# Optimization experiments

Hardware: AMD Instinct MI355X
Metric: run time of the kernel (lower is better)

Reference implementation:

```python
import jax, jax.numpy as jnp
import numpy as np

N = 50000
E = 800000
IN_C = 64
OUT_C = 128
T = 4


def setup_inputs() -> dict:
    key = jax.random.key(0)
    ks = jax.random.split(key, 12)
    s = 0.05
    return {
        "x": jax.random.normal(ks[0], (N, IN_C), dtype=jnp.float32),
        "u": jax.random.normal(ks[1], (N, OUT_C), dtype=jnp.float32),
        "edge_index": jax.random.randint(ks[2], (2, E), 0, N, dtype=jnp.int32),
        # w1: Linear(in_channels, out_channels)
        "w1_W": jax.random.normal(ks[3], (OUT_C, IN_C), dtype=jnp.float32) * s,
        "w1_b": jnp.zeros((OUT_C,), dtype=jnp.float32),
        # sigmod MLP: three Linear(out, out) layers
        "m1_W": jax.random.normal(ks[4], (OUT_C, OUT_C), dtype=jnp.float32) * s,
        "m1_b": jnp.zeros((OUT_C,), dtype=jnp.float32),
        "m2_W": jax.random.normal(ks[5], (OUT_C, OUT_C), dtype=jnp.float32) * s,
        "m2_b": jnp.zeros((OUT_C,), dtype=jnp.float32),
        "m3_W": jax.random.normal(ks[6], (OUT_C, OUT_C), dtype=jnp.float32) * s,
        "m3_b": jnp.zeros((OUT_C,), dtype=jnp.float32),
        # w2: Linear(out, out) for graph readout
        "w2_W": jax.random.normal(ks[7], (OUT_C, OUT_C), dtype=jnp.float32) * s,
        "w2_b": jnp.zeros((OUT_C,), dtype=jnp.float32),
    }


def reference(x, u, edge_index, w1_W, w1_b, m1_W, m1_b, m2_W, m2_b, m3_W, m3_b, w2_W, w2_b):
    n_nodes = x.shape[0]
    src = edge_index[0]  # gather source (u_j)
    dst = edge_index[1]  # scatter-add target
    xw = x @ w1_W.T + w1_b  # [N, out]; identical every iteration
    for _ in range(T):
        agg = jax.ops.segment_sum(u[src], dst, num_segments=n_nodes)  # [N, out]
        h = jax.nn.relu(agg @ m1_W.T + m1_b)
        h = jax.nn.relu(h @ m2_W.T + m2_b)
        h = jnp.tanh(h @ m3_W.T + m3_b)
        u = jax.nn.relu(xw + h)
    g = jnp.sum(u, axis=0, keepdims=True)  # e @ u with e = ones [1, N]
    return g @ w2_W.T + w2_b  # [1, out]
```

## Files before the change

kernel.cpp:

```cpp
#include <hip/hip_runtime.h>
#include <hip/hip_bf16.h>

#define NN 50000
#define NE 800000
#define CI 64
#define CO 128
#define SCANB 49

typedef __attribute__((ext_vector_type(8))) short bf16x8;
typedef __attribute__((ext_vector_type(4))) float f32x4;

__device__ __forceinline__ unsigned short f2bf(float f) {
  unsigned int u = __float_as_uint(f);
  u += 0x7fffu + ((u >> 16) & 1u);
  return (unsigned short)(u >> 16);
}
__device__ __forceinline__ float bf2f_lo(unsigned int p) { return __uint_as_float(p << 16); }
__device__ __forceinline__ float bf2f_hi(unsigned int p) { return __uint_as_float(p & 0xffff0000u); }
__device__ __forceinline__ unsigned int pk2(float lo, float hi) {
  return ((unsigned int)f2bf(hi) << 16) | (unsigned int)f2bf(lo);
}

__global__ void k_count(const int* __restrict__ dst, int* __restrict__ deg) {
  int e = blockIdx.x * blockDim.x + threadIdx.x;
  if (e < NE) atomicAdd(&deg[dst[e]], 1);
}

__global__ __launch_bounds__(256) void k_scan1(const int* __restrict__ deg, int* __restrict__ bsum) {
  int i0 = blockIdx.x * 1024 + threadIdx.x * 4;
  int s = 0;
#pragma unroll
  for (int j = 0; j < 4; ++j) { int i = i0 + j; if (i < NN) s += deg[i]; }
#pragma unroll
  for (int off = 32; off; off >>= 1) s += __shfl_down(s, off);
  __shared__ int ws[4];
  if ((threadIdx.x & 63) == 0) ws[threadIdx.x >> 6] = s;
  __syncthreads();
  if (threadIdx.x == 0) bsum[blockIdx.x] = ws[0] + ws[1] + ws[2] + ws[3];
}

__global__ __launch_bounds__(64) void k_scan2(const int* __restrict__ bsum, int* __restrict__ boff) {
  int t = threadIdx.x;
  int v = (t < SCANB) ? bsum[t] : 0;
  int incl = v;
#pragma unroll
  for (int off = 1; off < 64; off <<= 1) {
    int o = __shfl_up(incl, off);
    if (t >= off) incl += o;
  }
  if (t < SCANB) boff[t] = incl - v;
}

__global__ __launch_bounds__(256) void k_scan3(const int* __restrict__ deg, const int* __restrict__ boff,
                                               int* __restrict__ row_off) {
  int b = blockIdx.x;
  int i0 = b * 1024 + threadIdx.x * 4;
  int v[4]; int tsum = 0;
#pragma unroll
  for (int j = 0; j < 4; ++j) { int i = i0 + j; v[j] = (i < NN) ? deg[i] : 0; tsum += v[j]; }
  int incl = tsum;
#pragma unroll
  for (int off = 1; off < 64; off <<= 1) {
    int o = __shfl_up(incl, off);
    if ((threadIdx.x & 63) >= (unsigned)off) incl += o;
  }
  __shared__ int ws[4];
  int w = threadIdx.x >> 6;
  if ((threadIdx.x & 63) == 63) ws[w] = incl;
  __syncthreads();
  int wbase = 0;
  for (int k = 0; k < 4; ++k) if (k < w) wbase += ws[k];
  int excl = boff[b] + wbase + incl - tsum;
#pragma unroll
  for (int j = 0; j < 4; ++j) { int i = i0 + j; if (i < NN) row_off[i] = excl; excl += v[j]; }
  if (b == 0 && threadIdx.x == 0) row_off[NN] = NE;
}

__global__ void k_fill(const int* __restrict__ src, const int* __restrict__ dst,
                       const int* __restrict__ row_off, int* __restrict__ cursor,
                       int* __restrict__ ssrc) {
  int e = blockIdx.x * blockDim.x + threadIdx.x;
  if (e < NE) {
    int d = dst[e];
    int pos = atomicAdd(&cursor[d], 1);
    ssrc[row_off[d] + pos] = src[e];
  }
}

__global__ void k_cvt_w(const float* __restrict__ w1, const float* __restrict__ m1,
                        const float* __restrict__ m2, const float* __restrict__ m3,
                        unsigned short* __restrict__ o) {
  int i = blockIdx.x * blockDim.x + threadIdx.x;
  if (i >= 57344) return;
  float v;
  if (i < 8192) v = w1[i];
  else if (i < 24576) v = m1[i - 8192];
  else if (i < 40960) v = m2[i - 24576];
  else v = m3[i - 40960];
  o[i] = f2bf(v);
}

__global__ void k_cvt4(const float* __restrict__ in, unsigned short* __restrict__ out, int n4) {
  int i = blockIdx.x * blockDim.x + threadIdx.x;
  if (i >= n4) return;
  float4 v = *(const float4*)(in + i * 4);
  ushort2 lo = { f2bf(v.x), f2bf(v.y) };
  ushort2 hi = { f2bf(v.z), f2bf(v.w) };
  *(ushort2*)(out + i * 4) = lo;
  *(ushort2*)(out + i * 4 + 2) = hi;
}

__global__ __launch_bounds__(256) void k_gather(const int* __restrict__ row_off,
    const int* __restrict__ ssrc, const unsigned short* __restrict__ ubf,
    unsigned short* __restrict__ agg) {
  int node = blockIdx.x * 4 + (threadIdx.x >> 6);
  if (node >= NN) return;
  int lane = threadIdx.x & 63;
  int eg = lane >> 4, c = lane & 15;
  int beg = row_off[node], end = row_off[node + 1];
  float a[8];
#pragma unroll
  for (int i = 0; i < 8; ++i) a[i] = 0.f;

#define ADD8(r) { a[0] += bf2f_lo(r.x); a[1] += bf2f_hi(r.x); \
                  a[2] += bf2f_lo(r.y); a[3] += bf2f_hi(r.y); \
                  a[4] += bf2f_lo(r.z); a[5] += bf2f_hi(r.z); \
                  a[6] += bf2f_lo(r.w); a[7] += bf2f_hi(r.w); }

  for (int base = beg; base < end; base += 64) {
    int e = base + lane;
    int sid = (e < end) ? ssrc[e] : 0;
    int cnt = min(64, end - base);
    int j = 0;
    for (; j + 16 <= cnt; j += 16) {
      int s0 = __shfl(sid, j + 0 + eg);
      int s1 = __shfl(sid, j + 4 + eg);
      int s2 = __shfl(sid, j + 8 + eg);
      int s3 = __shfl(sid, j + 12 + eg);
      uint4 r0 = *(const uint4*)(ubf + (size_t)s0 * CO + c * 8);
      uint4 r1 = *(const uint4*)(ubf + (size_t)s1 * CO + c * 8);
      uint4 r2 = *(const uint4*)(ubf + (size_t)s2 * CO + c * 8);
      uint4 r3 = *(const uint4*)(ubf + (size_t)s3 * CO + c * 8);
      ADD8(r0); ADD8(r1); ADD8(r2); ADD8(r3);
    }
    for (; j + 4 <= cnt; j += 4) {
      int s = __shfl(sid, j + eg);
      uint4 r = *(const uint4*)(ubf + (size_t)s * CO + c * 8);
      ADD8(r);
    }
    if (j < cnt) {
      int rem = cnt - j;
      int s = __shfl(sid, j + min(eg, rem - 1));
      if (eg < rem) {
        uint4 r = *(const uint4*)(ubf + (size_t)s * CO + c * 8);
        ADD8(r);
      }
    }
  }
#undef ADD8
#pragma unroll
  for (int i = 0; i < 8; ++i) { a[i] += __shfl_xor(a[i], 16); a[i] += __shfl_xor(a[i], 32); }
  if (lane < 16) {
    uint4 o;
    o.x = pk2(a[0], a[1]); o.y = pk2(a[2], a[3]);
    o.z = pk2(a[4], a[5]); o.w = pk2(a[6], a[7]);
    *(uint4*)(agg + (size_t)node * CO + c * 8) = o;
  }
}

__global__ __launch_bounds__(256) void k_xw(const unsigned short* __restrict__ A,
    const unsigned short* __restrict__ W, const float* __restrict__ bias,
    unsigned short* __restrict__ xwb) {
  int wave = threadIdx.x >> 6, lane = threadIdx.x & 63;
  int m = lane & 15, q = lane >> 4;
  int row0 = blockIdx.x * 64 + wave * 16;
  int arow = row0 + m; if (arow >= NN) arow = NN - 1;
  const unsigned short* Ar = A + (size_t)arow * CI;
  f32x4 acc[8];
#pragma unroll
  for (int tt = 0; tt < 8; ++tt) acc[tt] = (f32x4){0.f, 0.f, 0.f, 0.f};
#pragma unroll
  for (int ks = 0; ks < CI; ks += 32) {
    bf16x8 a = *(const bf16x8*)(Ar + ks + q * 8);
#pragma unroll
    for (int tt = 0; tt < 8; ++tt) {
      bf16x8 b = *(const bf16x8*)(W + (size_t)(tt * 16 + m) * CI + ks + q * 8);
      acc[tt] = __builtin_amdgcn_mfma_f32_16x16x32_bf16(a, b, acc[tt], 0, 0, 0);
    }
  }
#pragma unroll
  for (int tt = 0; tt < 8; ++tt) {
    int o = tt * 16 + m;
    float bv = bias[o];
#pragma unroll
    for (int r = 0; r < 4; ++r) {
      int node = row0 + q * 4 + r;
      if (node < NN) xwb[(size_t)node * CO + o] = f2bf(acc[tt][r] + bv);
    }
  }
}

__global__ __launch_bounds__(512, 4) void k_mlp(const unsigned short* __restrict__ agg,
    const unsigned short* __restrict__ W1, const unsigned short* __restrict__ W2,
    const unsigned short* __restrict__ W3,
    const float* __restrict__ b1, const float* __restrict__ b2, const float* __restrict__ b3,
    const unsigned short* __restrict__ xwb, unsigned short* __restrict__ uout) {
  constexpr int SP = 136;
  __shared__ unsigned short lds[16384 + 8 * 16 * SP];
  unsigned short* wt = lds;
  int tid = threadIdx.x;
  int wave = tid >> 6, lane = tid & 63;
  int m = lane & 15, q = lane >> 4;
  int row0 = blockIdx.x * 128 + wave * 16;
  unsigned short* L = lds + 16384 + wave * 16 * SP;
  int ar = row0 + m; if (ar >= NN) ar = NN - 1;
  const unsigned short* Ap = agg + (size_t)ar * CO;

  uint4 wreg[4];
  const int trb = (tid >> 4) & 7;
  const int tc  = tid & 15;
  const int ldst0 = (tid >> 4) * 128 + ((tc ^ trb) << 3);
  auto stage_load = [&](const unsigned short* W) {
#pragma unroll
    for (int j = 0; j < 4; ++j)
      wreg[j] = *(const uint4*)(W + ((j * 512 + tid) << 3));
  };
  auto stage_write = [&]() {
#pragma unroll
    for (int j = 0; j < 4; ++j)
      *(uint4*)(wt + ldst0 + j * 4096) = wreg[j];
  };
  auto bfrag = [&](int t, int ks) -> bf16x8 {
    int ch = (ks >> 3) + q;
    return *(const bf16x8*)(wt + (t * 16 + m) * 128 + ((ch ^ (m & 7)) << 3));
  };

  stage_load(W1);
  bf16x8 ar4[4];
#pragma unroll
  for (int k4 = 0; k4 < 4; ++k4) ar4[k4] = *(const bf16x8*)(Ap + k4 * 32 + q * 8);
  stage_write();

  f32x4 acc[8];
#pragma unroll
  for (int t = 0; t < 8; ++t) acc[t] = (f32x4){0.f, 0.f, 0.f, 0.f};
  __syncthreads();

#pragma unroll
  for (int k4 = 0; k4 < 4; ++k4) {
#pragma unroll
    for (int t = 0; t < 8; ++t) {
      bf16x8 b = bfrag(t, k4 * 32);
      acc[t] = __builtin_amdgcn_mfma_f32_16x16x32_bf16(ar4[k4], b, acc[t], 0, 0, 0);
    }
  }
  stage_load(W2);
#pragma unroll
  for (int t = 0; t < 8; ++t) {
    float bv = b1[t * 16 + m];
#pragma unroll
    for (int r = 0; r < 4; ++r)
      L[(q * 4 + r) * SP + t * 16 + m] = f2bf(fmaxf(acc[t][r] + bv, 0.f));
  }
  __syncthreads();
  stage_write();
#pragma unroll
  for (int t = 0; t < 8; ++t) acc[t] = (f32x4){0.f, 0.f, 0.f, 0.f};
  __syncthreads();

#pragma unroll
  for (int ks = 0; ks < CO; ks += 32) {
    bf16x8 a = *(const bf16x8*)(L + m * SP + ks + q * 8);
#pragma unroll
    for (int t = 0; t < 8; ++t) {
      bf16x8 b = bfrag(t, ks);
      acc[t] = __builtin_amdgcn_mfma_f32_16x16x32_bf16(a, b, acc[t], 0, 0, 0);
    }
  }
  stage_load(W3);
#pragma unroll
  for (int t = 0; t < 8; ++t) {
    float bv = b2[t * 16 + m];
#pragma unroll
    for (int r = 0; r < 4; ++r)
      L[(q * 4 + r) * SP + t * 16 + m] = f2bf(fmaxf(acc[t][r] + bv, 0.f));
  }
  __syncthreads();
  stage_write();
#pragma unroll
  for (int t = 0; t < 8; ++t) acc[t] = (f32x4){0.f, 0.f, 0.f, 0.f};
  __syncthreads();

#pragma unroll
  for (int ks = 0; ks < CO; ks += 32) {
    bf16x8 a = *(const bf16x8*)(L + m * SP + ks + q * 8);
#pragma unroll
    for (int t = 0; t < 8; ++t) {
      bf16x8 b = bfrag(t, ks);
      acc[t] = __builtin_amdgcn_mfma_f32_16x16x32_bf16(a, b, acc[t], 0, 0, 0);
    }
  }
#pragma unroll
  for (int t = 0; t < 8; ++t) {
    float bv = b3[t * 16 + m];
#pragma unroll
    for (int r = 0; r < 4; ++r) {
      float v = acc[t][r] + bv;
      float e = __expf(2.f * v);
      v = 1.f - 2.f / (e + 1.f);
      L[(q * 4 + r) * SP + t * 16 + m] = f2bf(v);
    }
  }
  int ln = lane >> 2, lc = lane & 3;
  int gnode = row0 + ln;
  if (gnode < NN) {
    const unsigned short* xr = xwb + (size_t)gnode * CO;
    unsigned short* ur = uout + (size_t)gnode * CO;
#pragma unroll
    for (int rnd = 0; rnd < 4; ++rnd) {
      int ch = (rnd * 4 + lc) * 8;
      uint4 h = *(const uint4*)(L + ln * SP + ch);
      uint4 xv = *(const uint4*)(xr + ch);
      uint4 o;
      o.x = pk2(fmaxf(bf2f_lo(h.x) + bf2f_lo(xv.x), 0.f), fmaxf(bf2f_hi(h.x) + bf2f_hi(xv.x), 0.f));
      o.y = pk2(fmaxf(bf2f_lo(h.y) + bf2f_lo(xv.y), 0.f), fmaxf(bf2f_hi(h.y) + bf2f_hi(xv.y), 0.f));
      o.z = pk2(fmaxf(bf2f_lo(h.z) + bf2f_lo(xv.z), 0.f), fmaxf(bf2f_hi(h.z) + bf2f_hi(xv.z), 0.f));
      o.w = pk2(fmaxf(bf2f_lo(h.w) + bf2f_lo(xv.w), 0.f), fmaxf(bf2f_hi(h.w) + bf2f_hi(xv.w), 0.f));
      *(uint4*)(ur + ch) = o;
    }
  }
}

__global__ __launch_bounds__(256) void k_reduce(const unsigned short* __restrict__ u,
                                                float* __restrict__ g) {
  int ch2 = threadIdx.x & 63;
  int sub = threadIdx.x >> 6;
  float a0 = 0.f, a1 = 0.f;
  for (int n = blockIdx.x * 4 + sub; n < NN; n += gridDim.x * 4) {
    unsigned int p = *(const unsigned int*)(u + (size_t)n * CO + ch2 * 2);
    a0 += bf2f_lo(p); a1 += bf2f_hi(p);
  }
  __shared__ float s0[256], s1[256];
  s0[threadIdx.x] = a0; s1[threadIdx.x] = a1;
  __syncthreads();
  if (sub == 0) {
    a0 = s0[ch2] + s0[64 + ch2] + s0[128 + ch2] + s0[192 + ch2];
    a1 = s1[ch2] + s1[64 + ch2] + s1[128 + ch2] + s1[192 + ch2];
    atomicAdd(&g[ch2 * 2], a0);
    atomicAdd(&g[ch2 * 2 + 1], a1);
  }
}

__global__ void k_final(const float* __restrict__ g, const float* __restrict__ w2,
                        const float* __restrict__ b2, float* __restrict__ outp) {
  __shared__ float sg[128];
  if (threadIdx.x < 128) sg[threadIdx.x] = g[threadIdx.x];
  __syncthreads();
  int j = threadIdx.x;
  if (j < 128) {
    float acc = b2[j];
    for (int c = 0; c < 128; ++c) acc += sg[c] * w2[j * 128 + c];
    outp[j] = acc;
  }
}

extern "C" void kernel_launch(void* const* d_in, const int* in_sizes, int n_in,
                              void* d_out, int out_size, void* d_ws, size_t ws_size,
                              hipStream_t stream) {
  (void)in_sizes; (void)n_in; (void)out_size; (void)ws_size;
  const float* x   = (const float*)d_in[0];
  const float* u0  = (const float*)d_in[1];
  const int*   ei  = (const int*)d_in[2];
  const float* w1W = (const float*)d_in[3];
  const float* w1b = (const float*)d_in[4];
  const float* m1W = (const float*)d_in[5];
  const float* m1b = (const float*)d_in[6];
  const float* m2W = (const float*)d_in[7];
  const float* m2b = (const float*)d_in[8];
  const float* m3W = (const float*)d_in[9];
  const float* m3b = (const float*)d_in[10];
  const float* w2W = (const float*)d_in[11];
  const float* w2b = (const float*)d_in[12];
  const int* esrc = ei;
  const int* edst = ei + NE;

  char* p = (char*)d_ws;
  auto carve = [&](size_t bytes) { char* r = p; p += (bytes + 255) & ~(size_t)255; return r; };
  unsigned short* xwb     = (unsigned short*)carve((size_t)NN * CO * 2);
  unsigned short* ubf     = (unsigned short*)carve((size_t)NN * CO * 2);
  unsigned short* agg     = (unsigned short*)carve((size_t)NN * CO * 2);
  unsigned short* xb      = (unsigned short*)carve((size_t)NN * CI * 2);
  unsigned short* wbf     = (unsigned short*)carve((size_t)57344 * 2);
  int*            row_off = (int*)carve((size_t)(NN + 1) * 4);
  int*            deg     = (int*)carve((size_t)NN * 4);
  int*            cursor  = (int*)carve((size_t)NN * 4);
  int*            ssrc    = (int*)carve((size_t)NE * 4);
  int*            bsum    = (int*)carve((size_t)SCANB * 4);
  int*            boff    = (int*)carve((size_t)SCANB * 4);
  float*          g       = (float*)carve(128 * 4);

  hipMemsetAsync(deg, 0, (size_t)NN * 4, stream);
  hipMemsetAsync(cursor, 0, (size_t)NN * 4, stream);
  hipMemsetAsync(g, 0, 128 * 4, stream);

  k_count<<<(NE + 255) / 256, 256, 0, stream>>>(edst, deg);
  k_scan1<<<SCANB, 256, 0, stream>>>(deg, bsum);
  k_scan2<<<1, 64, 0, stream>>>(bsum, boff);
  k_scan3<<<SCANB, 256, 0, stream>>>(deg, boff, row_off);
  k_fill<<<(NE + 255) / 256, 256, 0, stream>>>(esrc, edst, row_off, cursor, ssrc);
  k_cvt_w<<<(57344 + 255) / 256, 256, 0, stream>>>(w1W, m1W, m2W, m3W, wbf);
  k_cvt4<<<(NN * CI / 4 + 255) / 256, 256, 0, stream>>>(x, xb, NN * CI / 4);
  k_cvt4<<<(NN * CO / 4 + 255) / 256, 256, 0, stream>>>(u0, ubf, NN * CO / 4);

  k_xw<<<(NN + 63) / 64, 256, 0, stream>>>(xb, wbf, w1b, xwb);

  const unsigned short* Wm1 = wbf + 8192;
  const unsigned short* Wm2 = wbf + 8192 + 16384;
  const unsigned short* Wm3 = wbf + 8192 + 2 * 16384;
  const int GM = (NN + 127) / 128;
  for (int it = 0; it < 4; ++it) {
    k_gather<<<(NN + 3) / 4, 256, 0, stream>>>(row_off, ssrc, ubf, agg);
    k_mlp<<<GM, 512, 0, stream>>>(agg, Wm1, Wm2, Wm3, m1b, m2b, m3b, xwb, ubf);
  }

  k_reduce<<<256, 256, 0, stream>>>(ubf, g);
  k_final<<<1, 128, 0, stream>>>(g, w2W, w2b, (float*)d_out);
}
```

Baseline: 450.1 us.

## Build CSR via two-level bucketing with LDS atomics instead of global atomics

Replaces the global-atomic degree count and scatter fill with a bucketed approach. Edges are first binned into 196 buckets of 256 destination nodes each, using block-local histograms and LDS atomics. Per-bucket kernels then compute degrees and fill the CSR source array using shared-memory counters. This removes contended and random global atomics, at the cost of more kernel launches, an extra pairs buffer, and low parallelism (196 blocks) in the per-bucket kernels.

```diff
diff --git a/kernel.cpp b/kernel.cpp
--- a/kernel.cpp
+++ b/kernel.cpp
@@ -6,6 +6,9 @@
 #define CI 64
 #define CO 128
 #define SCANB 49
+#define NB 196
+#define CHUNK 2048
+#define NCH 391
 
 typedef __attribute__((ext_vector_type(8))) short bf16x8;
 typedef __attribute__((ext_vector_type(4))) float f32x4;
@@ -21,9 +24,86 @@
   return ((unsigned int)f2bf(hi) << 16) | (unsigned int)f2bf(lo);
 }
 
-__global__ void k_count(const int* __restrict__ dst, int* __restrict__ deg) {
-  int e = blockIdx.x * blockDim.x + threadIdx.x;
-  if (e < NE) atomicAdd(&deg[dst[e]], 1);
+
+__global__ __launch_bounds__(256) void k_bhist(const int* __restrict__ dst,
+                                               int* __restrict__ bcnt) {
+  __shared__ int lc[NB];
+  int tid = threadIdx.x;
+  for (int t = tid; t < NB; t += 256) lc[t] = 0;
+  __syncthreads();
+  int base = blockIdx.x * CHUNK;
+#pragma unroll
+  for (int i = 0; i < 8; ++i) {
+    int idx = base + i * 256 + tid;
+    if (idx < NE) atomicAdd(&lc[dst[idx] >> 8], 1);
+  }
+  __syncthreads();
+  for (int t = tid; t < NB; t += 256) if (lc[t]) atomicAdd(&bcnt[t], lc[t]);
+}
+
+__global__ __launch_bounds__(256) void k_bscan(const int* __restrict__ bcnt,
+                                               int* __restrict__ bkt_off,
+                                               int* __restrict__ bkt_cur) {
+  __shared__ int s[256];
+  int t = threadIdx.x;
+  int v = (t < NB) ? bcnt[t] : 0;
+  s[t] = v;
+  __syncthreads();
+  for (int off = 1; off < 256; off <<= 1) {
+    int x = (t >= off) ? s[t - off] : 0;
+    __syncthreads();
+    s[t] += x;
+    __syncthreads();
+  }
+  if (t < NB) { int e = s[t] - v; bkt_off[t] = e; bkt_cur[t] = e; }
+  if (t == 0) bkt_off[NB] = NE;
+}
+
+__global__ __launch_bounds__(256) void k_bin(const int* __restrict__ src,
+                                             const int* __restrict__ dst,
+                                             int* __restrict__ bkt_cur,
+                                             uint2* __restrict__ pairs) {
+  __shared__ int lcnt[NB];
+  __shared__ int lbase[NB];
+  int tid = threadIdx.x;
+  for (int t = tid; t < NB; t += 256) lcnt[t] = 0;
+  __syncthreads();
+  int base = blockIdx.x * CHUNK;
+  int ds[8], sr[8], rk[8];
+#pragma unroll
+  for (int i = 0; i < 8; ++i) {
+    int idx = base + i * 256 + tid;
+    if (idx < NE) {
+      ds[i] = dst[idx]; sr[i] = src[idx];
+      rk[i] = atomicAdd(&lcnt[ds[i] >> 8], 1);
+    } else ds[i] = -1;
+  }
+  __syncthreads();
+  for (int t = tid; t < NB; t += 256)
+    lbase[t] = lcnt[t] ? atomicAdd(&bkt_cur[t], lcnt[t]) : 0;
+  __syncthreads();
+#pragma unroll
+  for (int i = 0; i < 8; ++i) {
+    if (ds[i] >= 0) {
+      uint2 pr; pr.x = (unsigned)sr[i]; pr.y = (unsigned)ds[i];
+      pairs[lbase[ds[i] >> 8] + rk[i]] = pr;
+    }
+  }
+}
+
+__global__ __launch_bounds__(256) void k_deg(const uint2* __restrict__ pairs,
+                                             const int* __restrict__ bkt_off,
+                                             int* __restrict__ deg) {
+  __shared__ int lc[256];
+  int t = threadIdx.x, b = blockIdx.x;
+  lc[t] = 0;
+  __syncthreads();
+  int beg = bkt_off[b], end = bkt_off[b + 1];
+  for (int i = beg + t; i < end; i += 256)
+    atomicAdd(&lc[pairs[i].y & 255], 1);
+  __syncthreads();
+  int node = (b << 8) + t;
+  if (node < NN) deg[node] = lc[t];
 }
 
 __global__ __launch_bounds__(256) void k_scan1(const int* __restrict__ deg, int* __restrict__ bsum) {
@@ -76,14 +156,20 @@
   if (b == 0 && threadIdx.x == 0) row_off[NN] = NE;
 }
 
-__global__ void k_fill(const int* __restrict__ src, const int* __restrict__ dst,
-                       const int* __restrict__ row_off, int* __restrict__ cursor,
-                       int* __restrict__ ssrc) {
-  int e = blockIdx.x * blockDim.x + threadIdx.x;
-  if (e < NE) {
-    int d = dst[e];
-    int pos = atomicAdd(&cursor[d], 1);
-    ssrc[row_off[d] + pos] = src[e];
+__global__ __launch_bounds__(256) void k_fillB(const uint2* __restrict__ pairs,
+                                               const int* __restrict__ bkt_off,
+                                               const int* __restrict__ row_off,
+                                               int* __restrict__ ssrc) {
+  __shared__ int lcur[256];
+  int t = threadIdx.x, b = blockIdx.x;
+  lcur[t] = 0;
+  __syncthreads();
+  int beg = bkt_off[b], end = bkt_off[b + 1];
+  for (int i = beg + t; i < end; i += 256) {
+    uint2 e = pairs[i];
+    int d = (int)e.y;
+    int pos = row_off[d] + atomicAdd(&lcur[d & 255], 1);
+    ssrc[pos] = (int)e.x;
   }
 }
 
@@ -393,21 +479,27 @@
   unsigned short* wbf     = (unsigned short*)carve((size_t)57344 * 2);
   int*            row_off = (int*)carve((size_t)(NN + 1) * 4);
   int*            deg     = (int*)carve((size_t)NN * 4);
-  int*            cursor  = (int*)carve((size_t)NN * 4);
   int*            ssrc    = (int*)carve((size_t)NE * 4);
+  uint2*          pairs   = (uint2*)carve((size_t)NE * 8);
+  int*            bkt_cnt = (int*)carve((size_t)NB * 4);
+  int*            bkt_off = (int*)carve((size_t)(NB + 1) * 4);
+  int*            bkt_cur = (int*)carve((size_t)NB * 4);
   int*            bsum    = (int*)carve((size_t)SCANB * 4);
   int*            boff    = (int*)carve((size_t)SCANB * 4);
   float*          g       = (float*)carve(128 * 4);
 
-  hipMemsetAsync(deg, 0, (size_t)NN * 4, stream);
-  hipMemsetAsync(cursor, 0, (size_t)NN * 4, stream);
+  hipMemsetAsync(bkt_cnt, 0, (size_t)NB * 4, stream);
   hipMemsetAsync(g, 0, 128 * 4, stream);
 
-  k_count<<<(NE + 255) / 256, 256, 0, stream>>>(edst, deg);
+  k_bhist<<<NCH, 256, 0, stream>>>(edst, bkt_cnt);
+  k_bscan<<<1, 256, 0, stream>>>(bkt_cnt, bkt_off, bkt_cur);
+  k_bin<<<NCH, 256, 0, stream>>>(esrc, edst, bkt_cur, pairs);
+  k_deg<<<NB, 256, 0, stream>>>(pairs, bkt_off, deg);
   k_scan1<<<SCANB, 256, 0, stream>>>(deg, bsum);
   k_scan2<<<1, 64, 0, stream>>>(bsum, boff);
   k_scan3<<<SCANB, 256, 0, stream>>>(deg, boff, row_off);
-  k_fill<<<(NE + 255) / 256, 256, 0, stream>>>(esrc, edst, row_off, cursor, ssrc);
+  k_fillB<<<NB, 256, 0, stream>>>(pairs, bkt_off, row_off, ssrc);
+
   k_cvt_w<<<(57344 + 255) / 256, 256, 0, stream>>>(w1W, m1W, m2W, m3W, wbf);
   k_cvt4<<<(NN * CI / 4 + 255) / 256, 256, 0, stream>>>(x, xb, NN * CI / 4);
   k_cvt4<<<(NN * CO / 4 + 255) / 256, 256, 0, stream>>>(u0, ubf, NN * CO / 4);
```

Result: faster. 410.3 us (-8.9%).
